# Performance work log

Measured on AMD Instinct MI355X. Metric: run time of the kernel, lower is better.

Reference implementation:

```python
import jax, jax.numpy as jnp
import numpy as np

VOCAB, EMB, HID, LABELS = 50000, 300, 200, 10
B, S = 32, 512


def _gru_direction(emb, h0, w_ih, w_hh, b_ih, b_hh):
    """Run a GRUCell recurrence over time. emb: [B,S,E], h0: [B,H] -> [B,S,H].
    PyTorch GRUCell gate order: r, z, n."""
    # Precompute input projections for all timesteps (one big GEMM).
    gi = jnp.einsum('bse,ge->bsg', emb, w_ih) + b_ih  # [B,S,3H]
    gi = jnp.transpose(gi, (1, 0, 2))  # [S,B,3H] for scan
    H = h0.shape[-1]

    def step(h, gi_t):
        gh = h @ w_hh.T + b_hh  # [B,3H]
        i_r, i_z, i_n = gi_t[:, :H], gi_t[:, H:2 * H], gi_t[:, 2 * H:]
        h_r, h_z, h_n = gh[:, :H], gh[:, H:2 * H], gh[:, 2 * H:]
        r = jax.nn.sigmoid(i_r + h_r)
        z = jax.nn.sigmoid(i_z + h_z)
        n = jnp.tanh(i_n + r * h_n)
        h_new = (1.0 - z) * n + z * h
        return h_new, h_new

    _, hs = jax.lax.scan(step, h0, gi)  # hs: [S,B,H]
    return jnp.transpose(hs, (1, 0, 2))  # [B,S,H]


def setup_inputs() -> dict:
    key = jax.random.key(0)
    ks = jax.random.split(key, 14)
    sc = 0.05
    return {
        'text': jax.random.randint(ks[0], (B, S), 0, VOCAB),
        'embedding': jax.random.normal(ks[1], (VOCAB, EMB), jnp.float32) * sc,
        'w_ih_f': jax.random.normal(ks[2], (3 * HID, EMB), jnp.float32) * sc,
        'w_hh_f': jax.random.normal(ks[3], (3 * HID, HID), jnp.float32) * sc,
        'b_ih_f': jax.random.normal(ks[4], (3 * HID,), jnp.float32) * sc,
        'b_hh_f': jax.random.normal(ks[5], (3 * HID,), jnp.float32) * sc,
        'w_ih_b': jax.random.normal(ks[6], (3 * HID, EMB), jnp.float32) * sc,
        'w_hh_b': jax.random.normal(ks[7], (3 * HID, HID), jnp.float32) * sc,
        'b_ih_b': jax.random.normal(ks[8], (3 * HID,), jnp.float32) * sc,
        'b_hh_b': jax.random.normal(ks[9], (3 * HID,), jnp.float32) * sc,
        'lin_w': jax.random.normal(ks[10], (LABELS, 2 * HID), jnp.float32) * sc,
        'lin_b': jax.random.normal(ks[11], (LABELS,), jnp.float32) * sc,
        'h0_f': jax.random.uniform(ks[12], (B, HID), jnp.float32),
        'h0_b': jax.random.uniform(ks[13], (B, HID), jnp.float32),
    }


def reference(text, embedding, w_ih_f, w_hh_f, b_ih_f, b_hh_f,
              w_ih_b, w_hh_b, b_ih_b, b_hh_b, lin_w, lin_b, h0_f, h0_b):
    emb = embedding[text]  # [B,S,E]
    hid = w_hh_f.shape[-1]
    h0f = (h0_f - 0.5) / hid  # matches (rand-0.5)/hidden_unit
    h0b = (h0_b - 0.5) / hid
    out_f = _gru_direction(emb, h0f, w_ih_f, w_hh_f, b_ih_f, b_hh_f)
    # backward direction: iterate t = S-1 .. 0, outputs re-ordered to time order
    out_b = _gru_direction(emb[:, ::-1, :], h0b, w_ih_b, w_hh_b, b_ih_b, b_hh_b)[:, ::-1, :]
    out = jnp.concatenate([out_f, out_b], axis=2)  # [B,S,2H]
    preds = out @ lin_w.T + lin_b  # [B,S,LABELS]
    return preds
```

## Files before the change

kernel.cpp:

```cpp
#include <hip/hip_runtime.h>
#include <hip/hip_fp16.h>

typedef _Float16 h8 __attribute__((ext_vector_type(8)));
typedef _Float16 h4 __attribute__((ext_vector_type(4)));
typedef _Float16 h2 __attribute__((ext_vector_type(2)));
typedef float f4 __attribute__((ext_vector_type(4)));

#define EMB    300
#define HID    200
#define NR     600
#define KP     320
#define NPAD   1216
#define SEQ    512
#define MTOT   16384

#if defined(__has_builtin)
#if __has_builtin(__builtin_amdgcn_fdot2)
#define USE_FDOT2 1
#endif
#endif

__device__ __forceinline__ float fdot2f(h2 a, h2 b, float c) {
#ifdef USE_FDOT2
  return __builtin_amdgcn_fdot2(a, b, c, false);
#else
  return c + (float)a[0] * (float)b[0] + (float)a[1] * (float)b[1];
#endif
}

__device__ __forceinline__ float sigm(float x) { return 1.0f / (1.0f + __expf(-x)); }
__device__ __forceinline__ float tanhf_(float x) { return 1.0f - 2.0f / (1.0f + __expf(2.0f * x)); }

__global__ __launch_bounds__(256) void prep_kernel(
    const float* __restrict__ w_ih_f, const float* __restrict__ w_ih_b,
    const float* __restrict__ b_ih_f, const float* __restrict__ b_ih_b,
    const float* __restrict__ w_hh_f, const float* __restrict__ w_hh_b,
    _Float16* __restrict__ Wcvt, float* __restrict__ bias_cat,
    h2* __restrict__ Whh2) {
  int idx = blockIdx.x * 256 + threadIdx.x;
  if (idx < NPAD * KP) {
    int n = idx / KP, k = idx - n * KP;
    float v = 0.0f;
    if (k < EMB) {
      if (n < NR) v = w_ih_f[n * EMB + k];
      else if (n < 2 * NR) v = w_ih_b[(n - NR) * EMB + k];
    }
    Wcvt[idx] = (_Float16)v;
  }
  if (idx < NPAD) {
    float bv = 0.0f;
    if (idx < NR) bv = b_ih_f[idx];
    else if (idx < 2 * NR) bv = b_ih_b[idx - NR];
    bias_cat[idx] = bv;
  }
  if (idx < 2 * 100 * NR) {
    int d = idx / (100 * NR);
    int rem = idx - d * (100 * NR);
    int kk = rem / NR, r = rem - kk * NR;
    const float* w = d ? w_hh_b : w_hh_f;
    float w0 = w[r * HID + 2 * kk];
    float w1 = w[r * HID + 2 * kk + 1];
    Whh2[idx] = (h2){ (_Float16)w0, (_Float16)w1 };
  }
}

__global__ __launch_bounds__(512) void gi_gemm(
    const int* __restrict__ text, const float* __restrict__ emb,
    const _Float16* __restrict__ Wcvt, const float* __restrict__ bias_cat,
    __half* __restrict__ gi) {
  __shared__ _Float16 At[128][328];
  const int t = threadIdx.x;
  const int m0 = blockIdx.x * 128;
  {
    const int row = t >> 2;
    const int q = t & 3;
    const int tokid = text[m0 + row];
    const float4* ep = (const float4*)(emb + (size_t)tokid * EMB);
    for (int c4 = q; c4 < 75; c4 += 4) {
      float4 v = ep[c4];
      h4 hv = { (_Float16)v.x, (_Float16)v.y, (_Float16)v.z, (_Float16)v.w };
      *(h4*)&At[row][c4 * 4] = hv;
    }
    for (int c = 300 + q; c < 328; c += 4) At[row][c] = (_Float16)0.0f;
  }
  __syncthreads();

  const int wv = t >> 6, lane = t & 63;
  const int l15 = lane & 15, l4 = lane >> 4;
  const int nhalf = wv >> 2;
  const int ms0 = (wv & 3) * 2;
  const int r0 = ms0 * 16 + l15;
  const int r1 = r0 + 16;

  for (int c2 = 0; c2 < 2; ++c2) {
    const int nbase = nhalf * 38 + c2 * 19;
    f4 acc0[19], acc1[19];
#pragma unroll
    for (int i = 0; i < 19; ++i) { acc0[i] = (f4){0,0,0,0}; acc1[i] = (f4){0,0,0,0}; }
    for (int ks = 0; ks < 10; ++ks) {
      h8 a0 = *(const h8*)&At[r0][ks * 32 + l4 * 8];
      h8 a1 = *(const h8*)&At[r1][ks * 32 + l4 * 8];
#pragma unroll
      for (int i = 0; i < 19; ++i) {
        const h8* bp = (const h8*)(Wcvt + (size_t)((nbase + i) * 16 + l15) * KP + ks * 32 + l4 * 8);
        h8 bf = *bp;
        acc0[i] = __builtin_amdgcn_mfma_f32_16x16x32_f16(a0, bf, acc0[i], 0, 0, 0);
        acc1[i] = __builtin_amdgcn_mfma_f32_16x16x32_f16(a1, bf, acc1[i], 0, 0, 0);
      }
    }
#pragma unroll
    for (int i = 0; i < 19; ++i) {
      const int n = (nbase + i) * 16 + l15;
      const float bv = bias_cat[n];
#pragma unroll
      for (int j = 0; j < 4; ++j) {
        const int mA = m0 + ms0 * 16 + l4 * 4 + j;
        gi[(size_t)mA * NPAD + n] = (__half)(acc0[i][j] + bv);
        gi[(size_t)(mA + 16) * NPAD + n] = (__half)(acc1[i][j] + bv);
      }
    }
  }
}

__global__ __launch_bounds__(640, 2) void gru_rec(
    const h2* __restrict__ Whh2,
    const float* __restrict__ b_hh_f, const float* __restrict__ b_hh_b,
    const float* __restrict__ h0_f,  const float* __restrict__ h0_b,
    const __half* __restrict__ gi, __half* __restrict__ hs) {
  const int t = threadIdx.x;
  const int dir = blockIdx.x >> 5;
  const int b = blockIdx.x & 31;
  const float* bhh_g = dir ? b_hh_b : b_hh_f;
  const float* h0 = dir ? h0_b : h0_f;

  __shared__ __align__(16) _Float16 h_sh[208];
  __shared__ float y_lds[NR];
  __shared__ __align__(16) _Float16 gi_lds[2][608];

  const int r = t;
  const bool arow = (r < NR);
  const int rr = arow ? r : 0;

  h2 w[100];
  const h2* Wd = Whh2 + (size_t)dir * 100 * NR;
#pragma unroll
  for (int kk = 0; kk < 100; ++kk) w[kk] = Wd[kk * NR + rr];
  const float ybias = arow ? bhh_g[r] : 0.0f;

  float hreg = 0.0f;
  if (t < HID) {
    hreg = (h0[b * HID + t] - 0.5f) * (1.0f / (float)HID);
    h_sh[t] = (_Float16)hreg;
  }
  {
    const int s0 = dir ? (SEQ - 1) : 0;
    const h4* g0 = (const h4*)(gi + (size_t)(b * SEQ + s0) * NPAD + dir * NR);
    if (t < 150) ((h4*)gi_lds[0])[t] = g0[t];
  }
  __syncthreads();

  for (int st = 0; st < SEQ; ++st) {
    const int cur = st & 1, nxt = cur ^ 1;
    const int s = dir ? (SEQ - 1 - st) : st;
    h4 pf = (h4){(_Float16)0, (_Float16)0, (_Float16)0, (_Float16)0};
    const bool do_pf = (t < 150) && (st < SEQ - 1);
    if (do_pf) {
      const int sn = dir ? (SEQ - 2 - st) : (st + 1);
      pf = ((const h4*)(gi + (size_t)(b * SEQ + sn) * NPAD + dir * NR))[t];
    }
    float a0 = ybias, a1 = 0.0f, a2 = 0.0f, a3 = 0.0f;
#pragma unroll
    for (int j = 0; j < 25; ++j) {
      h8 hv = *(const h8*)&h_sh[j * 8];
      a0 = fdot2f(w[4 * j + 0], (h2){hv[0], hv[1]}, a0);
      a1 = fdot2f(w[4 * j + 1], (h2){hv[2], hv[3]}, a1);
      a2 = fdot2f(w[4 * j + 2], (h2){hv[4], hv[5]}, a2);
      a3 = fdot2f(w[4 * j + 3], (h2){hv[6], hv[7]}, a3);
    }
    if (arow) y_lds[r] = (a0 + a1) + (a2 + a3);
    __syncthreads();
    if (t < HID) {
      const _Float16* gih = gi_lds[cur];
      const float ir = (float)gih[t];
      const float iz = (float)gih[200 + t];
      const float inn = (float)gih[400 + t];
      const float rg = sigm(ir + y_lds[t]);
      const float zg = sigm(iz + y_lds[200 + t]);
      const float ng = tanhf_(inn + rg * y_lds[400 + t]);
      hreg = (1.0f - zg) * ng + zg * hreg;
      h_sh[t] = (_Float16)hreg;
      hs[(size_t)(b * SEQ + s) * 400 + dir * HID + t] = (__half)hreg;
    }
    if (do_pf) ((h4*)gi_lds[nxt])[t] = pf;
    __syncthreads();
  }
}

__global__ __launch_bounds__(256) void final_linear(
    const __half* __restrict__ hs, const float* __restrict__ lin_w,
    const float* __restrict__ lin_b, float* __restrict__ out) {
  __shared__ _Float16 hsl[64][400];
  __shared__ _Float16 lwl[10][400];
  const int t = threadIdx.x;
  const int m0 = blockIdx.x * 64;
  const ushort4* hp = (const ushort4*)(hs + (size_t)m0 * 400);
  for (int idx = t; idx < 64 * 100; idx += 256) {
    ushort4 v = hp[idx];
    const int row = idx / 100, c = idx - row * 100;
    *(ushort4*)&hsl[row][c * 4] = v;
  }
  for (int idx = t; idx < 10 * 400; idx += 256) {
    (&lwl[0][0])[idx] = (_Float16)lin_w[idx];
  }
  __syncthreads();
  for (int idx = t; idx < 640; idx += 256) {
    const int m = idx / 10, c = idx - (idx / 10) * 10;
    const h2* hr = (const h2*)hsl[m];
    const h2* wr = (const h2*)lwl[c];
    float acc = 0.0f;
#pragma unroll 8
    for (int kk = 0; kk < 200; ++kk) acc = fdot2f(hr[kk], wr[kk], acc);
    out[(size_t)(m0 + m) * 10 + c] = acc + lin_b[c];
  }
}

extern "C" void kernel_launch(void* const* d_in, const int* in_sizes, int n_in,
                              void* d_out, int out_size, void* d_ws, size_t ws_size,
                              hipStream_t stream) {
  const int*   text   = (const int*)d_in[0];
  const float* emb    = (const float*)d_in[1];
  const float* w_ih_f = (const float*)d_in[2];
  const float* w_hh_f = (const float*)d_in[3];
  const float* b_ih_f = (const float*)d_in[4];
  const float* b_hh_f = (const float*)d_in[5];
  const float* w_ih_b = (const float*)d_in[6];
  const float* w_hh_b = (const float*)d_in[7];
  const float* b_ih_b = (const float*)d_in[8];
  const float* b_hh_b = (const float*)d_in[9];
  const float* lin_w  = (const float*)d_in[10];
  const float* lin_b  = (const float*)d_in[11];
  const float* h0_f   = (const float*)d_in[12];
  const float* h0_b   = (const float*)d_in[13];
  float* out = (float*)d_out;

  char* ws = (char*)d_ws;
  _Float16* Wcvt     = (_Float16*)(ws);
  float*    bias_cat = (float*)(ws + 778240);
  __half*   gi       = (__half*)(ws + 783360);
  __half*   hs       = (__half*)(ws + 40629248);
  h2*       Whh2     = (h2*)(ws + 53736448);

  prep_kernel<<<dim3((NPAD * KP + 255) / 256), dim3(256), 0, stream>>>(
      w_ih_f, w_ih_b, b_ih_f, b_ih_b, w_hh_f, w_hh_b, Wcvt, bias_cat, Whh2);
  gi_gemm<<<dim3(MTOT / 128), dim3(512), 0, stream>>>(
      text, emb, Wcvt, bias_cat, gi);
  gru_rec<<<dim3(64), dim3(640), 0, stream>>>(
      Whh2, b_hh_f, b_hh_b, h0_f, h0_b, gi, hs);
  final_linear<<<dim3(MTOT / 64), dim3(256), 0, stream>>>(
      hs, lin_w, lin_b, out);
}
```

Baseline: 883.3 us.

## Split GRU recurrent matvec across thread quads with DPP reduction and pre-swizzled weights

Recurrent step now uses 512 threads. Each group of four threads owns five hidden-gate rows, and each thread covers a quarter of the K dimension using row-major fp16 weights held in registers. Partial sums are combined with DPP quad shuffles. This shortens per-thread dependency chains and cuts per-step LDS reads of the hidden state from 25 vectors to 7. Separately, the input-projection weights are pre-laid out in MFMA fragment order for single coalesced loads, and the gi buffer drops its padded columns to reduce write traffic. In exchange each thread does more dot instructions, pays extra shuffle latency, and the zero-padded h tail makes the last quarter read neighbouring rows' weights multiplied by zero.

```diff
diff --git a/kernel.cpp b/kernel.cpp
--- a/kernel.cpp
+++ b/kernel.cpp
@@ -9,10 +9,11 @@
 #define EMB    300
 #define HID    200
 #define NR     600
-#define KP     320
-#define NPAD   1216
+#define GIS    1200
 #define SEQ    512
 #define MTOT   16384
+#define WROW_N 240000
+#define WROW_P 240032
 
 #if defined(__has_builtin)
 #if __has_builtin(__builtin_amdgcn_fdot2)
@@ -31,42 +32,51 @@
 __device__ __forceinline__ float sigm(float x) { return 1.0f / (1.0f + __expf(-x)); }
 __device__ __forceinline__ float tanhf_(float x) { return 1.0f - 2.0f / (1.0f + __expf(2.0f * x)); }
 
+__device__ __forceinline__ float qsum(float x) {
+  x += __int_as_float(__builtin_amdgcn_mov_dpp(__float_as_int(x), 0xB1, 0xF, 0xF, true));
+  x += __int_as_float(__builtin_amdgcn_mov_dpp(__float_as_int(x), 0x4E, 0xF, 0xF, true));
+  return x;
+}
+
 __global__ __launch_bounds__(256) void prep_kernel(
     const float* __restrict__ w_ih_f, const float* __restrict__ w_ih_b,
     const float* __restrict__ b_ih_f, const float* __restrict__ b_ih_b,
     const float* __restrict__ w_hh_f, const float* __restrict__ w_hh_b,
-    _Float16* __restrict__ Wcvt, float* __restrict__ bias_cat,
-    h2* __restrict__ Whh2) {
+    _Float16* __restrict__ Wfrag, float* __restrict__ bias_cat,
+    _Float16* __restrict__ Wrow) {
   int idx = blockIdx.x * 256 + threadIdx.x;
-  if (idx < NPAD * KP) {
-    int n = idx / KP, k = idx - n * KP;
+  if (idx < 76 * 10 * 64 * 8) {
+    int e = idx & 7, f = idx >> 3;
+    int lane = f & 63; f >>= 6;
+    int ks = f % 10, nt = f / 10;
+    int n = nt * 16 + (lane & 15);
+    int k = ks * 32 + (lane >> 4) * 8 + e;
     float v = 0.0f;
     if (k < EMB) {
       if (n < NR) v = w_ih_f[n * EMB + k];
       else if (n < 2 * NR) v = w_ih_b[(n - NR) * EMB + k];
     }
-    Wcvt[idx] = (_Float16)v;
-  }
-  if (idx < NPAD) {
+    Wfrag[idx] = (_Float16)v;
+  }
+  if (idx < 1216) {
     float bv = 0.0f;
     if (idx < NR) bv = b_ih_f[idx];
     else if (idx < 2 * NR) bv = b_ih_b[idx - NR];
     bias_cat[idx] = bv;
   }
-  if (idx < 2 * 100 * NR) {
-    int d = idx / (100 * NR);
-    int rem = idx - d * (100 * NR);
-    int kk = rem / NR, r = rem - kk * NR;
-    const float* w = d ? w_hh_b : w_hh_f;
-    float w0 = w[r * HID + 2 * kk];
-    float w1 = w[r * HID + 2 * kk + 1];
-    Whh2[idx] = (h2){ (_Float16)w0, (_Float16)w1 };
+  if (idx < WROW_P) {
+    float v = 0.0f;
+    if (idx < WROW_N) {
+      int d = idx / 120000, rem = idx - d * 120000;
+      v = (d ? w_hh_b : w_hh_f)[rem];
+    }
+    Wrow[idx] = (_Float16)v;
   }
 }
 
 __global__ __launch_bounds__(512) void gi_gemm(
     const int* __restrict__ text, const float* __restrict__ emb,
-    const _Float16* __restrict__ Wcvt, const float* __restrict__ bias_cat,
+    const _Float16* __restrict__ Wfrag, const float* __restrict__ bias_cat,
     __half* __restrict__ gi) {
   __shared__ _Float16 At[128][328];
   const int t = threadIdx.x;
@@ -102,8 +112,7 @@
       h8 a1 = *(const h8*)&At[r1][ks * 32 + l4 * 8];
 #pragma unroll
       for (int i = 0; i < 19; ++i) {
-        const h8* bp = (const h8*)(Wcvt + (size_t)((nbase + i) * 16 + l15) * KP + ks * 32 + l4 * 8);
-        h8 bf = *bp;
+        h8 bf = ((const h8*)Wfrag)[((size_t)(nbase + i) * 10 + ks) * 64 + lane];
         acc0[i] = __builtin_amdgcn_mfma_f32_16x16x32_f16(a0, bf, acc0[i], 0, 0, 0);
         acc1[i] = __builtin_amdgcn_mfma_f32_16x16x32_f16(a1, bf, acc1[i], 0, 0, 0);
       }
@@ -111,19 +120,37 @@
 #pragma unroll
     for (int i = 0; i < 19; ++i) {
       const int n = (nbase + i) * 16 + l15;
-      const float bv = bias_cat[n];
-#pragma unroll
-      for (int j = 0; j < 4; ++j) {
-        const int mA = m0 + ms0 * 16 + l4 * 4 + j;
-        gi[(size_t)mA * NPAD + n] = (__half)(acc0[i][j] + bv);
-        gi[(size_t)(mA + 16) * NPAD + n] = (__half)(acc1[i][j] + bv);
+      if (n < GIS) {
+        const float bv = bias_cat[n];
+#pragma unroll
+        for (int j = 0; j < 4; ++j) {
+          const int mA = m0 + ms0 * 16 + l4 * 4 + j;
+          gi[(size_t)mA * GIS + n] = (__half)(acc0[i][j] + bv);
+          gi[(size_t)(mA + 16) * GIS + n] = (__half)(acc1[i][j] + bv);
+        }
       }
     }
   }
 }
 
-__global__ __launch_bounds__(640, 2) void gru_rec(
-    const h2* __restrict__ Whh2,
+#define DOT8(w, x, A, B)                                        \
+  A = fdot2f((h2){(w)[0],(w)[1]}, (h2){(x)[0],(x)[1]}, A);      \
+  B = fdot2f((h2){(w)[2],(w)[3]}, (h2){(x)[2],(x)[3]}, B);      \
+  A = fdot2f((h2){(w)[4],(w)[5]}, (h2){(x)[4],(x)[5]}, A);      \
+  B = fdot2f((h2){(w)[6],(w)[7]}, (h2){(x)[6],(x)[7]}, B);
+
+#define ROW_VARS(i) h8 w##i##0, w##i##1, w##i##2, w##i##3, w##i##4, w##i##5, w##i##6
+#define ROW_LOAD(i) do { const h8* p = (const h8*)(Wrow + wbase + (size_t)(i) * 200); \
+  w##i##0 = p[0]; w##i##1 = p[1]; w##i##2 = p[2]; w##i##3 = p[3];                     \
+  w##i##4 = p[4]; w##i##5 = p[5]; w##i##6 = p[6]; } while (0)
+#define ROW_DOT(i, A, B) do {                                   \
+  DOT8(w##i##0, x0, A, B); DOT8(w##i##1, x1, A, B);             \
+  DOT8(w##i##2, x2, A, B); DOT8(w##i##3, x3, A, B);             \
+  DOT8(w##i##4, x4, A, B); DOT8(w##i##5, x5, A, B);             \
+  DOT8(w##i##6, x6, A, B); } while (0)
+
+__global__ __launch_bounds__(512, 1) void gru_rec(
+    const _Float16* __restrict__ Wrow,
     const float* __restrict__ b_hh_f, const float* __restrict__ b_hh_b,
     const float* __restrict__ h0_f,  const float* __restrict__ h0_b,
     const __half* __restrict__ gi, __half* __restrict__ hs) {
@@ -133,31 +160,32 @@
   const float* bhh_g = dir ? b_hh_b : b_hh_f;
   const float* h0 = dir ? h0_b : h0_f;
 
-  __shared__ __align__(16) _Float16 h_sh[208];
+  __shared__ __align__(16) _Float16 h_sh[224];
   __shared__ float y_lds[NR];
   __shared__ __align__(16) _Float16 gi_lds[2][608];
 
-  const int r = t;
-  const bool arow = (r < NR);
-  const int rr = arow ? r : 0;
-
-  h2 w[100];
-  const h2* Wd = Whh2 + (size_t)dir * 100 * NR;
-#pragma unroll
-  for (int kk = 0; kk < 100; ++kk) w[kk] = Wd[kk * NR + rr];
-  const float ybias = arow ? bhh_g[r] : 0.0f;
-
-  float hreg = 0.0f;
+  const int rg = t >> 2, kq = t & 3;
+  const bool arow = (rg < 120);
+  const int rbase = arow ? rg * 5 : 0;
+  const size_t wbase = (size_t)dir * 120000 + (size_t)rbase * 200 + 56 * kq;
+
+  ROW_VARS(0); ROW_VARS(1); ROW_VARS(2); ROW_VARS(3); ROW_VARS(4);
+  ROW_LOAD(0); ROW_LOAD(1); ROW_LOAD(2); ROW_LOAD(3); ROW_LOAD(4);
+
+  float bb0 = 0, bb1 = 0, bb2 = 0, hreg = 0;
   if (t < HID) {
+    bb0 = bhh_g[t]; bb1 = bhh_g[200 + t]; bb2 = bhh_g[400 + t];
     hreg = (h0[b * HID + t] - 0.5f) * (1.0f / (float)HID);
-    h_sh[t] = (_Float16)hreg;
-  }
+  }
+  if (t < 224) h_sh[t] = (t < HID) ? (_Float16)hreg : (_Float16)0.0f;
   {
     const int s0 = dir ? (SEQ - 1) : 0;
-    const h4* g0 = (const h4*)(gi + (size_t)(b * SEQ + s0) * NPAD + dir * NR);
+    const h4* g0 = (const h4*)(gi + (size_t)(b * SEQ + s0) * GIS + dir * NR);
     if (t < 150) ((h4*)gi_lds[0])[t] = g0[t];
   }
   __syncthreads();
+
+  const h8* hh = (const h8*)&h_sh[56 * kq];
 
   for (int st = 0; st < SEQ; ++st) {
     const int cur = st & 1, nxt = cur ^ 1;
@@ -166,27 +194,28 @@
     const bool do_pf = (t < 150) && (st < SEQ - 1);
     if (do_pf) {
       const int sn = dir ? (SEQ - 2 - st) : (st + 1);
-      pf = ((const h4*)(gi + (size_t)(b * SEQ + sn) * NPAD + dir * NR))[t];
-    }
-    float a0 = ybias, a1 = 0.0f, a2 = 0.0f, a3 = 0.0f;
-#pragma unroll
-    for (int j = 0; j < 25; ++j) {
-      h8 hv = *(const h8*)&h_sh[j * 8];
-      a0 = fdot2f(w[4 * j + 0], (h2){hv[0], hv[1]}, a0);
-      a1 = fdot2f(w[4 * j + 1], (h2){hv[2], hv[3]}, a1);
-      a2 = fdot2f(w[4 * j + 2], (h2){hv[4], hv[5]}, a2);
-      a3 = fdot2f(w[4 * j + 3], (h2){hv[6], hv[7]}, a3);
-    }
-    if (arow) y_lds[r] = (a0 + a1) + (a2 + a3);
+      pf = ((const h4*)(gi + (size_t)(b * SEQ + sn) * GIS + dir * NR))[t];
+    }
+    h8 x0 = hh[0], x1 = hh[1], x2 = hh[2], x3 = hh[3], x4 = hh[4], x5 = hh[5], x6 = hh[6];
+    float a0A = 0, a0B = 0, a1A = 0, a1B = 0, a2A = 0, a2B = 0,
+          a3A = 0, a3B = 0, a4A = 0, a4B = 0;
+    ROW_DOT(0, a0A, a0B); ROW_DOT(1, a1A, a1B); ROW_DOT(2, a2A, a2B);
+    ROW_DOT(3, a3A, a3B); ROW_DOT(4, a4A, a4B);
+    const float s0 = qsum(a0A + a0B), s1 = qsum(a1A + a1B), s2 = qsum(a2A + a2B),
+                s3 = qsum(a3A + a3B), s4 = qsum(a4A + a4B);
+    if (arow) {
+      y_lds[rbase + kq] = (kq == 0) ? s0 : (kq == 1) ? s1 : (kq == 2) ? s2 : s3;
+      if (kq == 0) y_lds[rbase + 4] = s4;
+    }
     __syncthreads();
     if (t < HID) {
       const _Float16* gih = gi_lds[cur];
       const float ir = (float)gih[t];
       const float iz = (float)gih[200 + t];
       const float inn = (float)gih[400 + t];
-      const float rg = sigm(ir + y_lds[t]);
-      const float zg = sigm(iz + y_lds[200 + t]);
-      const float ng = tanhf_(inn + rg * y_lds[400 + t]);
+      const float rgt = sigm(ir + y_lds[t] + bb0);
+      const float zg = sigm(iz + y_lds[200 + t] + bb1);
+      const float ng = tanhf_(inn + rgt * (y_lds[400 + t] + bb2));
       hreg = (1.0f - zg) * ng + zg * hreg;
       h_sh[t] = (_Float16)hreg;
       hs[(size_t)(b * SEQ + s) * 400 + dir * HID + t] = (__half)hreg;
@@ -244,18 +273,18 @@
   float* out = (float*)d_out;
 
   char* ws = (char*)d_ws;
-  _Float16* Wcvt     = (_Float16*)(ws);
+  _Float16* Wfrag    = (_Float16*)(ws);
   float*    bias_cat = (float*)(ws + 778240);
   __half*   gi       = (__half*)(ws + 783360);
-  __half*   hs       = (__half*)(ws + 40629248);
-  h2*       Whh2     = (h2*)(ws + 53736448);
-
-  prep_kernel<<<dim3((NPAD * KP + 255) / 256), dim3(256), 0, stream>>>(
-      w_ih_f, w_ih_b, b_ih_f, b_ih_b, w_hh_f, w_hh_b, Wcvt, bias_cat, Whh2);
+  _Float16* Wrow     = (_Float16*)(ws + 40104960);
+  __half*   hs       = (__half*)(ws + 40585088);
+
+  prep_kernel<<<dim3(1520), dim3(256), 0, stream>>>(
+      w_ih_f, w_ih_b, b_ih_f, b_ih_b, w_hh_f, w_hh_b, Wfrag, bias_cat, Wrow);
   gi_gemm<<<dim3(MTOT / 128), dim3(512), 0, stream>>>(
-      text, emb, Wcvt, bias_cat, gi);
-  gru_rec<<<dim3(64), dim3(640), 0, stream>>>(
-      Whh2, b_hh_f, b_hh_b, h0_f, h0_b, gi, hs);
+      text, emb, Wfrag, bias_cat, gi);
+  gru_rec<<<dim3(64), dim3(512), 0, stream>>>(
+      Wrow, b_hh_f, b_hh_b, h0_f, h0_b, gi, hs);
   final_linear<<<dim3(MTOT / 64), dim3(256), 0, stream>>>(
       hs, lin_w, lin_b, out);
 }
```

Measured after the change: 726.0 us. -17.8%, faster.
